# Kernel optimization log

Measured on AMD Instinct MI355X. Metric: run time of the kernel, lower is better.

Reference implementation:

```python
import jax, jax.numpy as jnp
import numpy as np
from jax import lax

BN_EPS = 1e-5


def _bn(t, g, b, m, v):
    # eval-mode BatchNorm2d over channel axis 1
    scale = (g / jnp.sqrt(v + BN_EPS))[None, :, None, None]
    return (t - m[None, :, None, None]) * scale + b[None, :, None, None]


def _conv1x1(t, w):
    # w: (out_c, in_c)
    return jnp.einsum('bchw,oc->bohw', t, w)


def setup_inputs() -> dict:
    key = jax.random.key(0)
    ks = jax.random.split(key, 8)
    B, C_in, H, W = 16, 640, 32, 32
    x = jax.random.normal(ks[0], (B, C_in, H, W), dtype=jnp.float32)

    def bn_params(k, c):
        k1, k2, k3, k4 = jax.random.split(k, 4)
        return (jax.random.normal(k1, (c,), jnp.float32) * 0.1 + 1.0,  # gamma
                jax.random.normal(k2, (c,), jnp.float32) * 0.1,        # beta
                jax.random.normal(k3, (c,), jnp.float32) * 0.1,        # running mean
                jax.random.uniform(k4, (c,), jnp.float32) + 0.5)       # running var

    bn1_g, bn1_b, bn1_m, bn1_v = bn_params(ks[1], 640)
    w_in = jax.random.normal(ks[2], (64, 640), jnp.float32) / np.sqrt(640)
    bnin_g, bnin_b, bnin_m, bnin_v = bn_params(ks[3], 64)
    w_emb = jax.random.normal(ks[4], (640, 1664), jnp.float32) / np.sqrt(1664)
    bne_g, bne_b, bne_m, bne_v = bn_params(ks[5], 640)
    w_out = jax.random.normal(ks[6], (640, 640), jnp.float32) / np.sqrt(640)
    bno_g, bno_b, bno_m, bno_v = bn_params(ks[7], 640)

    return dict(x=x,
                bn1_g=bn1_g, bn1_b=bn1_b, bn1_m=bn1_m, bn1_v=bn1_v,
                w_in=w_in, bnin_g=bnin_g, bnin_b=bnin_b, bnin_m=bnin_m, bnin_v=bnin_v,
                w_emb=w_emb, bne_g=bne_g, bne_b=bne_b, bne_m=bne_m, bne_v=bne_v,
                w_out=w_out, bno_g=bno_g, bno_b=bno_b, bno_m=bno_m, bno_v=bno_v)


def reference(x,
              bn1_g, bn1_b, bn1_m, bn1_v,
              w_in, bnin_g, bnin_b, bnin_m, bnin_v,
              w_emb, bne_g, bne_b, bne_m, bne_v,
              w_out, bno_g, bno_b, bno_m, bno_v):
    KH, KW = 5, 5
    x = jax.nn.relu(_bn(x, bn1_g, bn1_b, bn1_m, bn1_v))
    x = jax.nn.relu(_bn(_conv1x1(x, w_in), bnin_g, bnin_b, bnin_m, bnin_v))
    x0 = jax.nn.relu(x)  # second ReLU in original forward (no-op but faithful)
    # F.normalize(x, dim=1, p=2), eps=1e-12 (PyTorch default)
    norm = jnp.sqrt(jnp.sum(x0 * x0, axis=1, keepdims=True))
    identity = x0 / jnp.maximum(norm, 1e-12)
    b, c, h, w = identity.shape
    # unfold: (b, c*KH*KW, h, w), channel-major ordering matches torch Unfold
    patches = lax.conv_general_dilated_patches(
        identity, (KH, KW), (1, 1), ((2, 2), (2, 2)))
    corr = patches.reshape(b, c, KH * KW, h, w) * identity[:, :, None, :, :]
    corr = corr.reshape(b, c * KH * KW, h, w)
    # featureL2Norm: sqrt(sum(x^2, 1) + 1e-6)
    gs = corr / jnp.sqrt(jnp.sum(corr * corr, axis=1, keepdims=True) + 1e-6)
    feat = jnp.concatenate([identity, gs], axis=1)  # (b, 1664, h, w)
    e = jax.nn.relu(_bn(_conv1x1(feat, w_emb), bne_g, bne_b, bne_m, bne_v))
    out = _bn(_conv1x1(e, w_out), bno_g, bno_b, bno_m, bno_v)
    # dropout in eval mode = identity
    return out
```

## Files before the change

kernel.cpp:

```cpp
#include <hip/hip_runtime.h>
#include <math.h>

#define BN_EPS 1e-5f

using short8  = __attribute__((ext_vector_type(8))) short;
using f32x16  = __attribute__((ext_vector_type(16))) float;


__device__ __forceinline__ float bflo(unsigned u) { return __uint_as_float(u << 16); }
__device__ __forceinline__ float bfhi(unsigned u) { return __uint_as_float(u & 0xffff0000u); }

__device__ __forceinline__ unsigned bf16_rne(float f) {
    unsigned u = __float_as_uint(f);
    return (u + 0x7fffu + ((u >> 16) & 1u)) >> 16;
}
__device__ __forceinline__ unsigned pack_bf16(float lo, float hi) {
    return bf16_rne(lo) | (bf16_rne(hi) << 16);
}
__device__ __forceinline__ unsigned pk_hu(float lo, float hi) {
    unsigned a = __float_as_uint(lo) + 0x8000u;
    unsigned b = __float_as_uint(hi) + 0x8000u;
    return __builtin_amdgcn_perm(b, a, 0x07060302u);
}
__device__ __forceinline__ unsigned pmul_fast(unsigned a, unsigned b) {
    return pk_hu(bflo(a) * bflo(b), bfhi(a) * bfhi(b));
}

__global__ __launch_bounds__(256)
void k_prepAll(const float* __restrict__ x,
               const float* __restrict__ g1, const float* __restrict__ b1,
               const float* __restrict__ m1, const float* __restrict__ v1,
               const float* __restrict__ w_in,
               const float* __restrict__ gi, const float* __restrict__ bi,
               const float* __restrict__ mi, const float* __restrict__ vi,
               const float* __restrict__ w_emb,
               const float* __restrict__ ge, const float* __restrict__ be,
               const float* __restrict__ me, const float* __restrict__ ve,
               const float* __restrict__ w_out,
               const float* __restrict__ go, const float* __restrict__ bo,
               const float* __restrict__ mo, const float* __restrict__ vo,
               float* __restrict__ biasI, float* __restrict__ biasE, float* __restrict__ biasO,
               unsigned* __restrict__ wIt, unsigned* __restrict__ wEt, unsigned* __restrict__ wOt,
               unsigned* __restrict__ xpk)
{
    __shared__ float row[1664];
    const int tid = threadIdx.x;

    if (blockIdx.x >= 872) {
        __shared__ float scb[64];
        const int id2 = blockIdx.x - 872;
        const int b = id2 / 80;
        const int rem = id2 - b * 80;
        const int kc = rem >> 2, qr = rem & 3;
        const int p = qr * 256 + tid;
        if (tid < 64) {
            int ch = kc * 32 + (tid & 31);
            float s = g1[ch] * rsqrtf(v1[ch] + BN_EPS);
            scb[tid] = (tid < 32) ? s : (b1[ch] - m1[ch] * s);
        }
        __syncthreads();
        const float* xb = x + ((size_t)b * 640 + kc * 32) * 1024 + p;
        unsigned d[16];
#pragma unroll
        for (int j = 0; j < 16; j++) {
            float v0 = fmaxf(fmaf(xb[(size_t)(2 * j) * 1024],     scb[2 * j],     scb[32 + 2 * j]),     0.f);
            float v1_ = fmaxf(fmaf(xb[(size_t)(2 * j + 1) * 1024], scb[2 * j + 1], scb[32 + 2 * j + 1]), 0.f);
            d[j] = pack_bf16(v0, v1_);
        }
        char* dst = (char*)xpk + ((size_t)(b * 20 + kc) * 1024 + p) * 64;
#pragma unroll
        for (int o = 0; o < 4; o++)
            *(uint4*)(dst + o * 16) = make_uint4(d[4 * o], d[4 * o + 1], d[4 * o + 2], d[4 * o + 3]);
        return;
    }

    if (blockIdx.x < 640) {
        const int oc = blockIdx.x;
#pragma unroll
        for (int it = 0; it < 2; it++) {
            int u = it * 256 + tid;
            if (u < 416)
                ((float4*)row)[u] = ((const float4*)&w_emb[(size_t)oc * 1664])[u];
        }
        __syncthreads();
        if (tid < 208) {
            int kc = tid >> 2, kh = (tid >> 1) & 1, ksub = tid & 1;
            int k0 = kc * 32 + kh * 16 + ksub * 8;
            float sc = ge[oc] * rsqrtf(ve[oc] + BN_EPS);
            float v[8];
#pragma unroll
            for (int j = 0; j < 8; j++) {
                int kgp = k0 + j;
                int orig;
                if (kgp < 64) orig = kgp;
                else { int t = kgp - 64; orig = 64 + (t & 63) * 25 + (t >> 6); }
                v[j] = row[orig] * sc;
            }
            int mt = oc >> 7, mf = (oc >> 5) & 3;
            int idx = (mt * 52 + kc) * 512 + (mf * 2 + kh) * 64 + ksub * 32 + (oc & 31);
            ((uint4*)wEt)[idx] = make_uint4(pack_bf16(v[0], v[1]), pack_bf16(v[2], v[3]),
                                            pack_bf16(v[4], v[5]), pack_bf16(v[6], v[7]));
        }
        return;
    }

    int i = (blockIdx.x - 640) * 256 + tid;

    if (i < 64) {
        int c = i;
        float s = gi[c] * rsqrtf(vi[c] + BN_EPS);
        biasI[c] = bi[c] - mi[c] * s;
    } else if (i >= 704 && i < 1344) {
        int c = i - 704;
        float s = ge[c] * rsqrtf(ve[c] + BN_EPS);
        biasE[c] = be[c] - me[c] * s;
    } else if (i >= 1344 && i < 1984) {
        int c = i - 1344;
        float s = go[c] * rsqrtf(vo[c] + BN_EPS);
        biasO[c] = bo[c] - mo[c] * s;
    }

    if (i >= 2048 && i < 7168) {
        int u = i - 2048;
        int kc = u >> 8, w = u & 255;
        int mf = w >> 7, kh = (w >> 6) & 1, sl = w & 63;
        int oc = mf * 32 + (sl & 31);
        int k0 = kc * 32 + kh * 16 + (sl >> 5) * 8;
        float sc = gi[oc] * rsqrtf(vi[oc] + BN_EPS);
        unsigned d[4];
#pragma unroll
        for (int q = 0; q < 4; q++)
            d[q] = pack_bf16(w_in[oc * 640 + k0 + 2 * q] * sc,
                             w_in[oc * 640 + k0 + 2 * q + 1] * sc);
        ((uint4*)wIt)[u] = make_uint4(d[0], d[1], d[2], d[3]);
    }

    if (i >= 8192 && i < 59392) {
        int u = i - 8192;
        int ci = u >> 9, w = u & 511;
        int mt = ci / 20, kc = ci - mt * 20;
        int mf = w >> 7, kh = (w >> 6) & 1, sl = w & 63;
        int oc = mt * 128 + mf * 32 + (sl & 31);
        int k0 = kc * 32 + kh * 16 + (sl >> 5) * 8;
        float sc = go[oc] * rsqrtf(vo[oc] + BN_EPS);
        unsigned d[4];
#pragma unroll
        for (int q = 0; q < 4; q++)
            d[q] = pack_bf16(w_out[oc * 640 + k0 + 2 * q] * sc,
                             w_out[oc * 640 + k0 + 2 * q + 1] * sc);
        ((uint4*)wOt)[u] = make_uint4(d[0], d[1], d[2], d[3]);
    }
}

__device__ __forceinline__ uint4 gen_feat_unit(const short* slab, const short* ctrs,
                                               int kcAbs, int t)
{
    const int hf = t >> 7, sl = t & 63;
    const int bkh = (t >> 6) & 1;
    const int cl = bkh * 16 + (sl >> 5) * 8;
    if (kcAbs < 2) {
        int spxC = (hf + 2) * 36 + (sl & 31) + 2;
        return *(const uint4*)&slab[spxC * 72 + kcAbs * 32 + cl];
    } else {
        int pxl = hf * 32 + (sl & 31);
        int idx = kcAbs - 2;
        int ksp = idx >> 1;
        int cb = (idx & 1) * 32 + cl;
        int kho = ksp / 5, kwo = ksp - kho * 5;
        int spx = (hf + kho) * 36 + (sl & 31) + kwo;
        const unsigned* nb = (const unsigned*)&slab[spx * 72 + cb];
        const unsigned* ct = (const unsigned*)&ctrs[pxl * 72 + cb];
        return make_uint4(pmul_fast(nb[0], ct[0]), pmul_fast(nb[1], ct[1]),
                          pmul_fast(nb[2], ct[2]), pmul_fast(nb[3], ct[3]));
    }
}

__global__ __launch_bounds__(640, 3)
void k_mega(const unsigned* __restrict__ xpk,
            const unsigned* __restrict__ wIt, const float* __restrict__ biasI,
            const unsigned* __restrict__ wEt, const float* __restrict__ biasE,
            const unsigned* __restrict__ wOt, const float* __restrict__ biasO,
            float* __restrict__ out)
{
    __shared__ __align__(16) char Lds[106112];
    short* slab  = (short*)Lds;
    short* ctrs  = (short*)(Lds + 31104);
    float* invDs = (float*)(Lds + 40320);
    char*  stg   = Lds + 40576;
    uint4* Ep    = (uint4*)Lds;

    const int tid = threadIdx.x;
    const int l = tid & 63;
    const int w = tid >> 6;
    const int mt = w >> 1, mf0 = (w & 1) * 2;
    const int pt = blockIdx.x;
    const int b = pt >> 4, r0 = (pt & 15) * 2;

    if (w < 7) {
        const int spx = w * 32 + (l & 31);
        const int spxc = spx < 216 ? spx : 215;
        const int sr = spxc / 36, sc = spxc - sr * 36;
        const int r = r0 + sr - 2, cc = sc - 2;
        const bool valid = (spx < 216) && (r >= 0) && (r < 32) && (cc >= 0) && (cc < 32);
        const int rcl = min(max(r, 0), 31), ccl = min(max(cc, 0), 31);
        const int pcl = rcl * 32 + ccl;
        const char* xb = (const char*)xpk + ((size_t)b * 1310720 + (size_t)pcl * 64 + ((l >> 5) * 16));

        f32x16 accI[2];
#pragma unroll
        for (int i = 0; i < 2; i++)
#pragma unroll
            for (int rr = 0; rr < 16; rr++) accI[i][rr] = 0.f;

        uint4 bq[2], bqn[2], av[2][2], avn[2][2];
#pragma unroll
        for (int kh = 0; kh < 2; kh++)
            bq[kh] = *(const uint4*)(xb + kh * 32);
#pragma unroll
        for (int mi2 = 0; mi2 < 2; mi2++)
#pragma unroll
            for (int kh = 0; kh < 2; kh++)
                av[mi2][kh] = ((const uint4*)wIt)[(mi2 << 7) + (kh << 6) + l];

        for (int kc = 0; kc < 20; kc++) {
            if (kc < 19) {
#pragma unroll
                for (int kh = 0; kh < 2; kh++)
                    bqn[kh] = *(const uint4*)(xb + (size_t)(kc + 1) * 65536 + kh * 32);
#pragma unroll
                for (int mi2 = 0; mi2 < 2; mi2++)
#pragma unroll
                    for (int kh = 0; kh < 2; kh++)
                        avn[mi2][kh] = ((const uint4*)wIt)[(kc + 1) * 256 + (mi2 << 7) + (kh << 6) + l];
            }
#pragma unroll
            for (int kh = 0; kh < 2; kh++) {
                accI[0] = __builtin_amdgcn_mfma_f32_32x32x16_bf16(*(short8*)&av[0][kh], *(short8*)&bq[kh], accI[0], 0, 0, 0);
                accI[1] = __builtin_amdgcn_mfma_f32_32x32x16_bf16(*(short8*)&av[1][kh], *(short8*)&bq[kh], accI[1], 0, 0, 0);
            }
            if (kc < 19) {
#pragma unroll
                for (int kh = 0; kh < 2; kh++) bq[kh] = bqn[kh];
#pragma unroll
                for (int mi2 = 0; mi2 < 2; mi2++)
#pragma unroll
                    for (int kh = 0; kh < 2; kh++) av[mi2][kh] = avn[mi2][kh];
            }
        }
        float ss = 0.f;
#pragma unroll
        for (int mi2 = 0; mi2 < 2; mi2++)
#pragma unroll
            for (int rg = 0; rg < 4; rg++) {
                float4 bb = *(const float4*)&biasI[mi2 * 32 + 8 * rg + 4 * (l >> 5)];
#pragma unroll
                for (int q = 0; q < 4; q++) {
                    float bv = (q == 0) ? bb.x : (q == 1) ? bb.y : (q == 2) ? bb.z : bb.w;
                    float t = fmaxf(accI[mi2][rg * 4 + q] + bv, 0.f);
                    accI[mi2][rg * 4 + q] = t;
                    ss = fmaf(t, t, ss);
                }
            }
        ss += __shfl_xor(ss, 32);
        float inv = 1.f / fmaxf(sqrtf(ss), 1e-12f);
        if (spx < 216) {
#pragma unroll
            for (int mi2 = 0; mi2 < 2; mi2++)
#pragma unroll
                for (int rg = 0; rg < 4; rg++) {
                    unsigned d0 = pack_bf16(accI[mi2][rg * 4 + 0] * inv, accI[mi2][rg * 4 + 1] * inv);
                    unsigned d1 = pack_bf16(accI[mi2][rg * 4 + 2] * inv, accI[mi2][rg * 4 + 3] * inv);
                    if (!valid) { d0 = 0u; d1 = 0u; }
                    *(uint2*)&slab[spx * 72 + mi2 * 32 + 8 * rg + 4 * (l >> 5)] = make_uint2(d0, d1);
                }
        }
    }
    __syncthreads();

    if (tid < 512) {
        int px = tid >> 3, part = tid & 7;
        int rh = px >> 5, rw = px & 31;
        float ctr[8];
        const unsigned* cp = (const unsigned*)&slab[((rh + 2) * 36 + rw + 2) * 72 + part * 8];
#pragma unroll
        for (int d = 0; d < 4; d++) { ctr[2 * d] = bflo(cp[d]); ctr[2 * d + 1] = bfhi(cp[d]); }
        float sum = 0.f;
#pragma unroll
        for (int k = 0; k < 25; k++) {
            const int kh = k / 5, kw = k % 5;
            const unsigned* nb = (const unsigned*)&slab[((rh + kh) * 36 + rw + kw) * 72 + part * 8];
#pragma unroll
            for (int d = 0; d < 4; d++) {
                float q0 = bflo(nb[d]) * ctr[2 * d];
                float q1 = bfhi(nb[d]) * ctr[2 * d + 1];
                sum = fmaf(q0, q0, sum); sum = fmaf(q1, q1, sum);
            }
        }
        sum += __shfl_xor(sum, 1);
        sum += __shfl_xor(sum, 2);
        sum += __shfl_xor(sum, 4);
        if (part == 0) invDs[px] = rsqrtf(sum + 1e-6f);
    }
    __syncthreads();

    if (tid < 512) {
        int px = tid >> 3, q = tid & 7;
        int spx = ((px >> 5) + 2) * 36 + (px & 31) + 2;
        const unsigned* src = (const unsigned*)&slab[spx * 72 + q * 8];
        float iv = invDs[px];
        unsigned d[4];
#pragma unroll
        for (int dd = 0; dd < 4; dd++)
            d[dd] = pk_hu(bflo(src[dd]) * iv, bfhi(src[dd]) * iv);
        *(uint4*)&ctrs[px * 72 + q * 8] = make_uint4(d[0], d[1], d[2], d[3]);
    }
    __syncthreads();

    const uint4* A = (const uint4*)wEt + (size_t)(mt * 52) * 512;

    f32x16 acc[2][2];
#pragma unroll
    for (int i = 0; i < 2; i++)
#pragma unroll
        for (int j = 0; j < 2; j++)
#pragma unroll
            for (int r = 0; r < 16; r++) acc[i][j][r] = 0.f;

    uint4 avc[2][2];
#pragma unroll
    for (int mi = 0; mi < 2; mi++)
#pragma unroll
        for (int kh = 0; kh < 2; kh++)
            avc[mi][kh] = A[(((mf0 + mi) * 2 + kh) << 6) + l];

#pragma unroll
    for (int k = 0; k < 4; k++) {
        int u = tid + k * 640;
        if (u < 2048) {
            uint4 f = gen_feat_unit(slab, ctrs, (u >> 8), u & 255);
            *(uint4*)&stg[u * 16] = f;
        }
    }
    __syncthreads();

    uint4 bvc[2][2];
#pragma unroll
    for (int ni = 0; ni < 2; ni++)
#pragma unroll
        for (int kh = 0; kh < 2; kh++)
            bvc[ni][kh] = *(const uint4*)&stg[((ni << 7) + (kh << 6) + l) * 16];

#pragma unroll 1
    for (int c = 0; c < 6; c++) {
        const int cur = c & 1, nxt = cur ^ 1;
        const int base = c * 8;
        {
            const int nunits = (c < 5) ? 2048 : 1024;
            const int nbase = base + 8;
#pragma unroll
            for (int k = 0; k < 4; k++) {
                int u = tid + k * 640;
                if (u < nunits) {
                    uint4 f = gen_feat_unit(slab, ctrs, nbase + (u >> 8), u & 255);
                    *(uint4*)&stg[nxt * 32768 + u * 16] = f;
                }
            }
        }
#pragma unroll
        for (int kcL = 0; kcL < 8; kcL++) {
            const int kc = base + kcL;
            uint4 avn[2][2];
#pragma unroll
            for (int mi = 0; mi < 2; mi++)
#pragma unroll
                for (int kh = 0; kh < 2; kh++)
                    avn[mi][kh] = A[(size_t)(kc + 1) * 512 + (((mf0 + mi) * 2 + kh) << 6) + l];
            uint4 bvn[2][2];
            if (kcL < 7) {
#pragma unroll
                for (int ni = 0; ni < 2; ni++)
#pragma unroll
                    for (int kh = 0; kh < 2; kh++)
                        bvn[ni][kh] = *(const uint4*)&stg[cur * 32768 + ((kcL + 1) * 256 + (ni << 7) + (kh << 6) + l) * 16];
            }
#pragma unroll
            for (int kh = 0; kh < 2; kh++) {
                acc[0][0] = __builtin_amdgcn_mfma_f32_32x32x16_bf16(*(short8*)&avc[0][kh], *(short8*)&bvc[0][kh], acc[0][0], 0, 0, 0);
                acc[0][1] = __builtin_amdgcn_mfma_f32_32x32x16_bf16(*(short8*)&avc[0][kh], *(short8*)&bvc[1][kh], acc[0][1], 0, 0, 0);
                acc[1][0] = __builtin_amdgcn_mfma_f32_32x32x16_bf16(*(short8*)&avc[1][kh], *(short8*)&bvc[0][kh], acc[1][0], 0, 0, 0);
                acc[1][1] = __builtin_amdgcn_mfma_f32_32x32x16_bf16(*(short8*)&avc[1][kh], *(short8*)&bvc[1][kh], acc[1][1], 0, 0, 0);
            }
#pragma unroll
            for (int mi = 0; mi < 2; mi++)
#pragma unroll
                for (int kh = 0; kh < 2; kh++) avc[mi][kh] = avn[mi][kh];
            if (kcL < 7) {
#pragma unroll
                for (int ni = 0; ni < 2; ni++)
#pragma unroll
                    for (int kh = 0; kh < 2; kh++) bvc[ni][kh] = bvn[ni][kh];
            }
        }
        __syncthreads();
#pragma unroll
        for (int ni = 0; ni < 2; ni++)
#pragma unroll
            for (int kh = 0; kh < 2; kh++)
                bvc[ni][kh] = *(const uint4*)&stg[nxt * 32768 + ((ni << 7) + (kh << 6) + l) * 16];
    }
#pragma unroll
    for (int kcL = 0; kcL < 4; kcL++) {
        const int kc = 48 + kcL;
        uint4 avn[2][2], bvn[2][2];
        if (kcL < 3) {
#pragma unroll
            for (int mi = 0; mi < 2; mi++)
#pragma unroll
                for (int kh = 0; kh < 2; kh++)
                    avn[mi][kh] = A[(size_t)(kc + 1) * 512 + (((mf0 + mi) * 2 + kh) << 6) + l];
#pragma unroll
            for (int ni = 0; ni < 2; ni++)
#pragma unroll
                for (int kh = 0; kh < 2; kh++)
                    bvn[ni][kh] = *(const uint4*)&stg[((kcL + 1) * 256 + (ni << 7) + (kh << 6) + l) * 16];
        }
#pragma unroll
        for (int kh = 0; kh < 2; kh++) {
            acc[0][0] = __builtin_amdgcn_mfma_f32_32x32x16_bf16(*(short8*)&avc[0][kh], *(short8*)&bvc[0][kh], acc[0][0], 0, 0, 0);
            acc[0][1] = __builtin_amdgcn_mfma_f32_32x32x16_bf16(*(short8*)&avc[0][kh], *(short8*)&bvc[1][kh], acc[0][1], 0, 0, 0);
            acc[1][0] = __builtin_amdgcn_mfma_f32_32x32x16_bf16(*(short8*)&avc[1][kh], *(short8*)&bvc[0][kh], acc[1][0], 0, 0, 0);
            acc[1][1] = __builtin_amdgcn_mfma_f32_32x32x16_bf16(*(short8*)&avc[1][kh], *(short8*)&bvc[1][kh], acc[1][1], 0, 0, 0);
        }
        if (kcL < 3) {
#pragma unroll
            for (int mi = 0; mi < 2; mi++)
#pragma unroll
                for (int kh = 0; kh < 2; kh++) avc[mi][kh] = avn[mi][kh];
#pragma unroll
            for (int ni = 0; ni < 2; ni++)
#pragma unroll
                for (int kh = 0; kh < 2; kh++) bvc[ni][kh] = bvn[ni][kh];
        }
    }
    __syncthreads();

#pragma unroll
    for (int mi = 0; mi < 2; mi++) {
        const int kbase = (w * 2 + mi) * 256;
#pragma unroll
        for (int ni = 0; ni < 2; ni++) {
#pragma unroll
            for (int rg = 0; rg < 4; rg++) {
                int ocb = w * 64 + mi * 32 + 8 * rg + 4 * (l >> 5);
                float4 bb = *(const float4*)&biasE[ocb];
                unsigned d0 = pack_bf16(fmaxf(acc[mi][ni][rg * 4 + 0] + bb.x, 0.f),
                                        fmaxf(acc[mi][ni][rg * 4 + 1] + bb.y, 0.f));
                unsigned d1 = pack_bf16(fmaxf(acc[mi][ni][rg * 4 + 2] + bb.z, 0.f),
                                        fmaxf(acc[mi][ni][rg * 4 + 3] + bb.w, 0.f));
                int unit = kbase + (ni << 7) + ((rg >> 1) << 6) + ((rg & 1) << 5) + (l & 31);
                ((uint2*)Ep)[unit * 2 + (l >> 5)] = make_uint2(d0, d1);
            }
        }
    }
    __syncthreads();

    const int p0 = pt * 64;
    const int hw0 = p0 & 1023;
    const uint4* Ao = (const uint4*)wOt + (size_t)(mt * 20) * 512;

    f32x16 acc2[2][2];
#pragma unroll
    for (int i = 0; i < 2; i++)
#pragma unroll
        for (int j = 0; j < 2; j++)
#pragma unroll
            for (int r = 0; r < 16; r++) acc2[i][j][r] = 0.f;

    uint4 aoc[2][2], boc[2][2];
#pragma unroll
    for (int mi = 0; mi < 2; mi++)
#pragma unroll
        for (int kh = 0; kh < 2; kh++)
            aoc[mi][kh] = Ao[(((mf0 + mi) * 2 + kh) << 6) + l];
#pragma unroll
    for (int ni = 0; ni < 2; ni++)
#pragma unroll
        for (int kh = 0; kh < 2; kh++)
            boc[ni][kh] = Ep[(ni << 7) + (kh << 6) + l];

#pragma unroll 4
    for (int kc = 0; kc < 20; kc++) {
        uint4 aon[2][2], bon[2][2];
        if (kc < 19) {
#pragma unroll
            for (int mi = 0; mi < 2; mi++)
#pragma unroll
                for (int kh = 0; kh < 2; kh++)
                    aon[mi][kh] = Ao[(size_t)(kc + 1) * 512 + (((mf0 + mi) * 2 + kh) << 6) + l];
#pragma unroll
            for (int ni = 0; ni < 2; ni++)
#pragma unroll
                for (int kh = 0; kh < 2; kh++)
                    bon[ni][kh] = Ep[(kc + 1) * 256 + (ni << 7) + (kh << 6) + l];
        }
#pragma unroll
        for (int kh = 0; kh < 2; kh++) {
            acc2[0][0] = __builtin_amdgcn_mfma_f32_32x32x16_bf16(*(short8*)&aoc[0][kh], *(short8*)&boc[0][kh], acc2[0][0], 0, 0, 0);
            acc2[0][1] = __builtin_amdgcn_mfma_f32_32x32x16_bf16(*(short8*)&aoc[0][kh], *(short8*)&boc[1][kh], acc2[0][1], 0, 0, 0);
            acc2[1][0] = __builtin_amdgcn_mfma_f32_32x32x16_bf16(*(short8*)&aoc[1][kh], *(short8*)&boc[0][kh], acc2[1][0], 0, 0, 0);
            acc2[1][1] = __builtin_amdgcn_mfma_f32_32x32x16_bf16(*(short8*)&aoc[1][kh], *(short8*)&boc[1][kh], acc2[1][1], 0, 0, 0);
        }
        if (kc < 19) {
#pragma unroll
            for (int mi = 0; mi < 2; mi++)
#pragma unroll
                for (int kh = 0; kh < 2; kh++) aoc[mi][kh] = aon[mi][kh];
#pragma unroll
            for (int ni = 0; ni < 2; ni++)
#pragma unroll
                for (int kh = 0; kh < 2; kh++) boc[ni][kh] = bon[ni][kh];
        }
    }

#pragma unroll
    for (int mi = 0; mi < 2; mi++)
#pragma unroll
        for (int ni = 0; ni < 2; ni++) {
            int pxl = ni * 32 + (l & 31);
#pragma unroll
            for (int r = 0; r < 16; r++) {
                int oc = w * 64 + mi * 32 + (r & 3) + 8 * (r >> 2) + 4 * (l >> 5);
                out[((size_t)b * 640 + oc) * 1024 + hw0 + pxl] = acc2[mi][ni][r] + biasO[oc];
            }
        }
}

extern "C" void kernel_launch(void* const* d_in, const int* in_sizes, int n_in,
                              void* d_out, int out_size, void* d_ws, size_t ws_size,
                              hipStream_t stream)
{
    const float* x    = (const float*)d_in[0];
    const float* g1   = (const float*)d_in[1];
    const float* b1   = (const float*)d_in[2];
    const float* m1   = (const float*)d_in[3];
    const float* v1   = (const float*)d_in[4];
    const float* w_in = (const float*)d_in[5];
    const float* gi   = (const float*)d_in[6];
    const float* bi   = (const float*)d_in[7];
    const float* mi   = (const float*)d_in[8];
    const float* vi   = (const float*)d_in[9];
    const float* w_emb= (const float*)d_in[10];
    const float* ge   = (const float*)d_in[11];
    const float* be   = (const float*)d_in[12];
    const float* me   = (const float*)d_in[13];
    const float* ve   = (const float*)d_in[14];
    const float* w_out= (const float*)d_in[15];
    const float* go   = (const float*)d_in[16];
    const float* bo   = (const float*)d_in[17];
    const float* mo   = (const float*)d_in[18];
    const float* vo   = (const float*)d_in[19];

    char* ws = (char*)d_ws;
    float*    biasI = (float*)(ws + 5120);
    float*    biasE = (float*)(ws + 5376);
    float*    biasO = (float*)(ws + 7936);
    unsigned* wIt   = (unsigned*)(ws + 16384);
    unsigned* wOt   = (unsigned*)(ws + 98304);
    unsigned* wEt   = (unsigned*)(ws + 917504);
    unsigned* xpk   = (unsigned*)(ws + 3047424);
    float*    out   = (float*)d_out;

    k_prepAll<<<2152, 256, 0, stream>>>(x, g1, b1, m1, v1, w_in, gi, bi, mi, vi,
                                        w_emb, ge, be, me, ve, w_out, go, bo, mo, vo,
                                        biasI, biasE, biasO, wIt, wEt, wOt, xpk);
    k_mega<<<256, 640, 0, stream>>>(xpk, wIt, biasI,
                                    wEt, biasE, wOt, biasO, out);
}
```

Measured before the change: 192.5 us.

## Batch w_emb prep per block, swizzle mega-kernel tiles, deepen first GEMM prefetch

The w_emb transpose and pack step now handles 8 output channels per block instead of one, which cuts the prep grid from 2152 to 1592 blocks and raises shared-memory use to about 53KB. The mega kernel remaps blockIdx so consecutive blocks fall on different batch and row tiles, which changes how the work spreads across CUs and how it hits the cache. The first 1x1 conv loop is unrolled by two, with a double-buffered prefetch of x one K chunk further ahead, to hide global load latency. The extra live registers could strain occupancy at launch bounds (640,3).

Measured after the change: 190.0 us. No clear change (-1.3%).

```diff
diff --git a/kernel.cpp b/kernel.cpp
--- a/kernel.cpp
+++ b/kernel.cpp
@@ -43,12 +43,11 @@
                unsigned* __restrict__ wIt, unsigned* __restrict__ wEt, unsigned* __restrict__ wOt,
                unsigned* __restrict__ xpk)
 {
-    __shared__ float row[1664];
     const int tid = threadIdx.x;
 
-    if (blockIdx.x >= 872) {
+    if (blockIdx.x >= 312) {
         __shared__ float scb[64];
-        const int id2 = blockIdx.x - 872;
+        const int id2 = blockIdx.x - 312;
         const int b = id2 / 80;
         const int rem = id2 - b * 80;
         const int kc = rem >> 2, qr = rem & 3;
@@ -74,37 +73,50 @@
         return;
     }
 
-    if (blockIdx.x < 640) {
-        const int oc = blockIdx.x;
-#pragma unroll
-        for (int it = 0; it < 2; it++) {
+    if (blockIdx.x < 80) {
+        __shared__ float rows[8 * 1664];
+        __shared__ float scs[8];
+        const int oc0 = blockIdx.x * 8;
+#pragma unroll
+        for (int it = 0; it < 13; it++) {
             int u = it * 256 + tid;
-            if (u < 416)
-                ((float4*)row)[u] = ((const float4*)&w_emb[(size_t)oc * 1664])[u];
+            if (u < 3328)
+                ((float4*)rows)[u] = ((const float4*)w_emb)[(size_t)oc0 * 416 + u];
+        }
+        if (tid < 8) {
+            int oc = oc0 + tid;
+            scs[tid] = ge[oc] * rsqrtf(ve[oc] + BN_EPS);
         }
         __syncthreads();
-        if (tid < 208) {
-            int kc = tid >> 2, kh = (tid >> 1) & 1, ksub = tid & 1;
-            int k0 = kc * 32 + kh * 16 + ksub * 8;
-            float sc = ge[oc] * rsqrtf(ve[oc] + BN_EPS);
-            float v[8];
-#pragma unroll
-            for (int j = 0; j < 8; j++) {
-                int kgp = k0 + j;
-                int orig;
-                if (kgp < 64) orig = kgp;
-                else { int t = kgp - 64; orig = 64 + (t & 63) * 25 + (t >> 6); }
-                v[j] = row[orig] * sc;
-            }
-            int mt = oc >> 7, mf = (oc >> 5) & 3;
-            int idx = (mt * 52 + kc) * 512 + (mf * 2 + kh) * 64 + ksub * 32 + (oc & 31);
-            ((uint4*)wEt)[idx] = make_uint4(pack_bf16(v[0], v[1]), pack_bf16(v[2], v[3]),
-                                            pack_bf16(v[4], v[5]), pack_bf16(v[6], v[7]));
+#pragma unroll
+        for (int it = 0; it < 7; it++) {
+            int t = it * 256 + tid;
+            if (t < 1664) {
+                int ocl = t / 208, sub = t - ocl * 208;
+                int oc = oc0 + ocl;
+                int kc = sub >> 2, kh = (sub >> 1) & 1, ksub = sub & 1;
+                int k0 = kc * 32 + kh * 16 + ksub * 8;
+                float sc = scs[ocl];
+                const float* row = &rows[ocl * 1664];
+                float v[8];
+#pragma unroll
+                for (int j = 0; j < 8; j++) {
+                    int kgp = k0 + j;
+                    int orig;
+                    if (kgp < 64) orig = kgp;
+                    else { int tt = kgp - 64; orig = 64 + (tt & 63) * 25 + (tt >> 6); }
+                    v[j] = row[orig] * sc;
+                }
+                int mt = oc >> 7, mf = (oc >> 5) & 3;
+                int idx = (mt * 52 + kc) * 512 + (mf * 2 + kh) * 64 + ksub * 32 + (oc & 31);
+                ((uint4*)wEt)[idx] = make_uint4(pack_bf16(v[0], v[1]), pack_bf16(v[2], v[3]),
+                                                pack_bf16(v[4], v[5]), pack_bf16(v[6], v[7]));
+            }
         }
         return;
     }
 
-    int i = (blockIdx.x - 640) * 256 + tid;
+    int i = (blockIdx.x - 80) * 256 + tid;
 
     if (i < 64) {
         int c = i;
@@ -193,7 +205,8 @@
     const int l = tid & 63;
     const int w = tid >> 6;
     const int mt = w >> 1, mf0 = (w & 1) * 2;
-    const int pt = blockIdx.x;
+    const int bx = blockIdx.x;
+    const int pt = ((bx & 7) << 5) | (bx >> 3);
     const int b = pt >> 4, r0 = (pt & 15) * 2;
 
     if (w < 7) {
@@ -212,39 +225,50 @@
 #pragma unroll
             for (int rr = 0; rr < 16; rr++) accI[i][rr] = 0.f;
 
-        uint4 bq[2], bqn[2], av[2][2], avn[2][2];
-#pragma unroll
-        for (int kh = 0; kh < 2; kh++)
-            bq[kh] = *(const uint4*)(xb + kh * 32);
+        uint4 bq0[2], bq1[2], avA[2][2], avB[2][2];
+#pragma unroll
+        for (int kh = 0; kh < 2; kh++) {
+            bq0[kh] = *(const uint4*)(xb + kh * 32);
+            bq1[kh] = *(const uint4*)(xb + 65536 + kh * 32);
+        }
 #pragma unroll
         for (int mi2 = 0; mi2 < 2; mi2++)
 #pragma unroll
             for (int kh = 0; kh < 2; kh++)
-                av[mi2][kh] = ((const uint4*)wIt)[(mi2 << 7) + (kh << 6) + l];
-
-        for (int kc = 0; kc < 20; kc++) {
-            if (kc < 19) {
-#pragma unroll
-                for (int kh = 0; kh < 2; kh++)
-                    bqn[kh] = *(const uint4*)(xb + (size_t)(kc + 1) * 65536 + kh * 32);
+                avA[mi2][kh] = ((const uint4*)wIt)[(mi2 << 7) + (kh << 6) + l];
+
+#pragma unroll 1
+        for (int kc2 = 0; kc2 < 10; kc2++) {
+            const int kc = kc2 * 2;
+#pragma unroll
+            for (int mi2 = 0; mi2 < 2; mi2++)
+#pragma unroll
+                for (int kh = 0; kh < 2; kh++)
+                    avB[mi2][kh] = ((const uint4*)wIt)[(kc + 1) * 256 + (mi2 << 7) + (kh << 6) + l];
+#pragma unroll
+            for (int kh = 0; kh < 2; kh++) {
+                accI[0] = __builtin_amdgcn_mfma_f32_32x32x16_bf16(*(short8*)&avA[0][kh], *(short8*)&bq0[kh], accI[0], 0, 0, 0);
+                accI[1] = __builtin_amdgcn_mfma_f32_32x32x16_bf16(*(short8*)&avA[1][kh], *(short8*)&bq0[kh], accI[1], 0, 0, 0);
+            }
+            if (kc + 2 < 20) {
+#pragma unroll
+                for (int kh = 0; kh < 2; kh++)
+                    bq0[kh] = *(const uint4*)(xb + (size_t)(kc + 2) * 65536 + kh * 32);
 #pragma unroll
                 for (int mi2 = 0; mi2 < 2; mi2++)
 #pragma unroll
                     for (int kh = 0; kh < 2; kh++)
-                        avn[mi2][kh] = ((const uint4*)wIt)[(kc + 1) * 256 + (mi2 << 7) + (kh << 6) + l];
+                        avA[mi2][kh] = ((const uint4*)wIt)[(kc + 2) * 256 + (mi2 << 7) + (kh << 6) + l];
             }
 #pragma unroll
             for (int kh = 0; kh < 2; kh++) {
-                accI[0] = __builtin_amdgcn_mfma_f32_32x32x16_bf16(*(short8*)&av[0][kh], *(short8*)&bq[kh], accI[0], 0, 0, 0);
-                accI[1] = __builtin_amdgcn_mfma_f32_32x32x16_bf16(*(short8*)&av[1][kh], *(short8*)&bq[kh], accI[1], 0, 0, 0);
-            }
-            if (kc < 19) {
-#pragma unroll
-                for (int kh = 0; kh < 2; kh++) bq[kh] = bqn[kh];
-#pragma unroll
-                for (int mi2 = 0; mi2 < 2; mi2++)
-#pragma unroll
-                    for (int kh = 0; kh < 2; kh++) av[mi2][kh] = avn[mi2][kh];
+                accI[0] = __builtin_amdgcn_mfma_f32_32x32x16_bf16(*(short8*)&avB[0][kh], *(short8*)&bq1[kh], accI[0], 0, 0, 0);
+                accI[1] = __builtin_amdgcn_mfma_f32_32x32x16_bf16(*(short8*)&avB[1][kh], *(short8*)&bq1[kh], accI[1], 0, 0, 0);
+            }
+            if (kc + 3 < 20) {
+#pragma unroll
+                for (int kh = 0; kh < 2; kh++)
+                    bq1[kh] = *(const uint4*)(xb + (size_t)(kc + 3) * 65536 + kh * 32);
             }
         }
         float ss = 0.f;
@@ -570,7 +594,7 @@
     unsigned* xpk   = (unsigned*)(ws + 3047424);
     float*    out   = (float*)d_out;
 
-    k_prepAll<<<2152, 256, 0, stream>>>(x, g1, b1, m1, v1, w_in, gi, bi, mi, vi,
+    k_prepAll<<<1592, 256, 0, stream>>>(x, g1, b1, m1, v1, w_in, gi, bi, mi, vi,
                                         w_emb, ge, be, me, ve, w_out, go, bo, mo, vo,
                                         biasI, biasE, biasO, wIt, wEt, wOt, xpk);
     k_mega<<<256, 640, 0, stream>>>(xpk, wIt, biasI,
```
